# Kernel tuning notes

Hardware: AMD Instinct MI355X
Metric: run time of the kernel (lower is better)

The kernel has to match this reference:

```python
import jax, jax.numpy as jnp
import numpy as np

NUM_EMBEDDINGS = 1024
EMBEDDING_DIM = 256
COMMITMENT_COST = 0.25


def setup_inputs() -> dict:
    key = jax.random.key(0)
    k1, k2 = jax.random.split(key)
    x = jax.random.normal(k1, (16, 4096, EMBEDDING_DIM), dtype=jnp.float32)
    # torch init: uniform(-1/K, 1/K); keep same scale
    embedding_weight = jax.random.uniform(
        k2, (NUM_EMBEDDINGS, EMBEDDING_DIM), dtype=jnp.float32,
        minval=-1.0 / NUM_EMBEDDINGS, maxval=1.0 / NUM_EMBEDDINGS)
    return {"x": x, "embedding_weight": embedding_weight}


def reference(x, embedding_weight):
    original_shape = x.shape
    x_flat = x.reshape(-1, EMBEDDING_DIM)                     # [N, D]
    d2 = (jnp.sum(x_flat ** 2, axis=1, keepdims=True)
          + jnp.sum(embedding_weight ** 2, axis=1)
          - 2.0 * x_flat @ embedding_weight.T)                # [N, K]
    d2 = jnp.maximum(d2, 0.0)
    encoding_indices = jnp.argmin(d2, axis=1)                 # [N]
    quantized_flat = embedding_weight[encoding_indices]        # [N, D]
    quantized = quantized_flat.reshape(original_shape)

    q_sg = jax.lax.stop_gradient(quantized)
    codebook_loss = jnp.mean((q_sg - x) ** 2)
    commitment_loss = jnp.mean((x - q_sg) ** 2)
    vq_total_loss = codebook_loss + COMMITMENT_COST * commitment_loss

    # straight-through estimator
    quantized_st = x + jax.lax.stop_gradient(quantized - x)

    # perplexity via index counts (avoids materializing one-hot [N, K])
    n = x_flat.shape[0]
    counts = jnp.zeros((NUM_EMBEDDINGS,), jnp.float32).at[encoding_indices].add(1.0)
    avg_probs = counts / n
    perplexity = jnp.exp(-jnp.sum(avg_probs * jnp.log(avg_probs + 1e-10)))

    return quantized_st, vq_total_loss, perplexity, encoding_indices
```

## Files before the change

### kernel.cpp

```cpp
#include <hip/hip_runtime.h>
#include <math.h>

#define N_ROWS   65536
#define DIM      256
#define KCODES   1024
#define Q_SIZE   (N_ROWS * DIM)
#define OUT_LOSS Q_SIZE
#define OUT_PERP (Q_SIZE + 1)
#define OUT_IDX  (Q_SIZE + 2)

#define TAUP 200.0f

#define WS_LOSS   0
#define WS_RCNT   8
#define WS_E2     16
#define WS_E2P    4112
#define WS_COUNTS 8208
#define WS_IDX    12304
#define WS_RLIST  274448
#define WS_ET     536592
#define WS_P      1585168

typedef _Float16 half8 __attribute__((ext_vector_type(8)));
typedef _Float16 half4 __attribute__((ext_vector_type(4)));
typedef float    f32x4 __attribute__((ext_vector_type(4)));

#define ROWB 528
#define RPB  128

#define LDS_E2 49152

__global__ void k_prep(const float* __restrict__ E, float* __restrict__ e2,
                       float* __restrict__ e2p, float* __restrict__ Et,
                       _Float16* __restrict__ P,
                       int* __restrict__ counts, double* __restrict__ loss,
                       int* __restrict__ rcnt) {
    int b = blockIdx.x, t = threadIdx.x;
    __shared__ double red[256];
    float v = E[b * DIM + t];
    red[t] = (double)v * (double)v;

    {
        int o    = b * 256 + t;
        int j    = o & 7;
        int lane = (o >> 3) & 63;
        int c    = (o >> 9) & 15;
        int T    = o >> 13;
        int nt = c >> 3, kk = c & 7;
        int code = T * 32 + nt * 16 + (lane & 15);
        int d    = (lane >> 4) * 8 + kk * 32 + j;
        P[o] = (_Float16)(E[code * DIM + d] * 1024.0f);
    }

    __syncthreads();
    for (int s = 128; s > 0; s >>= 1) {
        if (t < s) red[t] += red[t + s];
        __syncthreads();
    }
    if (t == 0) { e2[b] = (float)red[0]; e2p[b] = (float)(red[0] * 1048576.0); }

    int o = b * 256 + t;
    int d = o >> 10, k = o & 1023;
    Et[o] = E[k * DIM + d];

    if (b < 4) counts[b * 256 + t] = 0;
    if (b == 0 && t == 0) { *loss = 0.0; *rcnt = 0; }
}

__global__ void __launch_bounds__(256)
k_main(const float* __restrict__ X, const _Float16* __restrict__ P,
       const float* __restrict__ e2p,
       int* __restrict__ idx_ws, int* __restrict__ rlist,
       int* __restrict__ rcnt) {
    __shared__ __align__(16) char sAll[53248];
    const int tid  = threadIdx.x;
    const int wid  = tid >> 6;
    const int lane = tid & 63;
    const int c16  = lane & 15;
    const int kg   = lane >> 4;
    const int rb   = blockIdx.x * RPB;

    char* sX = sAll;
    char* sB = sAll;
    const float* sE2 = (const float*)(sAll + LDS_E2);

    ((f32x4*)(sAll + LDS_E2))[tid] = ((const f32x4*)e2p)[tid];

    {
        const f32x4* Xg = (const f32x4*)(X + (size_t)rb * DIM);
        #pragma unroll
        for (int it = 0; it < 16; ++it) {
            int f = it * 256 + tid;
            int row = f >> 6, d4 = f & 63;
            f32x4 v = __builtin_nontemporal_load(&Xg[(size_t)row * 64 + d4]);
            half4 hh = {(_Float16)v[0], (_Float16)v[1], (_Float16)v[2], (_Float16)v[3]};
            *(half4*)(sX + row * ROWB + d4 * 8) = hh;
        }
    }
    __syncthreads();
    half8 ar[2][8];
    if (wid < 2) {
        #pragma unroll
        for (int mt = 0; mt < 2; ++mt)
            #pragma unroll
            for (int kk = 0; kk < 8; ++kk)
                ar[mt][kk] = *(const half8*)(sX + (wid * 32 + mt * 16 + c16) * ROWB
                                             + kk * 64 + kg * 16);
    }
    __syncthreads();
    {
        const f32x4* Xg = (const f32x4*)(X + (size_t)(rb + 64) * DIM);
        #pragma unroll
        for (int it = 0; it < 16; ++it) {
            int f = it * 256 + tid;
            int row = f >> 6, d4 = f & 63;
            f32x4 v = __builtin_nontemporal_load(&Xg[(size_t)row * 64 + d4]);
            half4 hh = {(_Float16)v[0], (_Float16)v[1], (_Float16)v[2], (_Float16)v[3]};
            *(half4*)(sX + row * ROWB + d4 * 8) = hh;
        }
    }
    __syncthreads();
    if (wid >= 2) {
        #pragma unroll
        for (int mt = 0; mt < 2; ++mt)
            #pragma unroll
            for (int kk = 0; kk < 8; ++kk)
                ar[mt][kk] = *(const half8*)(sX + ((wid - 2) * 32 + mt * 16 + c16) * ROWB
                                             + kk * 64 + kg * 16);
    }
    __syncthreads();

#define STAGE(T)                                                                             \
    {                                                                                        \
        const char* src_ = (const char*)P + (size_t)(T) * 16384 + (size_t)(wid * 4) * 1024   \
                           + (size_t)lane * 16;                                              \
        char* dst_ = sB + ((T) % 3) * 16384 + (wid * 4) * 1024;                              \
        __builtin_amdgcn_global_load_lds((const __attribute__((address_space(1))) unsigned int*)(src_),          \
                                         (__attribute__((address_space(3))) unsigned int*)(dst_), 16, 0, 0);     \
        __builtin_amdgcn_global_load_lds((const __attribute__((address_space(1))) unsigned int*)(src_ + 1024),   \
                                         (__attribute__((address_space(3))) unsigned int*)(dst_ + 1024), 16, 0, 0);\
        __builtin_amdgcn_global_load_lds((const __attribute__((address_space(1))) unsigned int*)(src_ + 2048),   \
                                         (__attribute__((address_space(3))) unsigned int*)(dst_ + 2048), 16, 0, 0);\
        __builtin_amdgcn_global_load_lds((const __attribute__((address_space(1))) unsigned int*)(src_ + 3072),   \
                                         (__attribute__((address_space(3))) unsigned int*)(dst_ + 3072), 16, 0, 0);\
    }
#define SB0 __builtin_amdgcn_sched_barrier(0)

    float tb1[8], tb2[8];
    int   ti1[8];
    #pragma unroll
    for (int i = 0; i < 8; ++i) { tb1[i] = 3.4e38f; tb2[i] = 3.4e38f; ti1[i] = 0; }

    f32x4 acc[2][2];

    STAGE(0); STAGE(1);
    SB0;

    #pragma unroll 2
    for (int T = 0; T < 32; ++T) {
        if (T <= 30) { asm volatile("s_waitcnt vmcnt(4)" ::: "memory"); }
        else         { asm volatile("s_waitcnt vmcnt(0)" ::: "memory"); }
        SB0;
        __builtin_amdgcn_s_barrier();
        SB0;
        if (T < 30) STAGE(T + 2);
        SB0;

        #pragma unroll
        for (int mt = 0; mt < 2; ++mt)
            #pragma unroll
            for (int nt = 0; nt < 2; ++nt) acc[mt][nt] = 0.0f;

        const char* bbuf = sB + (T % 3) * 16384 + (size_t)lane * 16;
        #pragma unroll
        for (int kk = 0; kk < 8; ++kk) {
            half8 b0 = *(const half8*)(bbuf + (0 * 8 + kk) * 1024);
            half8 b1 = *(const half8*)(bbuf + (1 * 8 + kk) * 1024);
            acc[0][0] = __builtin_amdgcn_mfma_f32_16x16x32_f16(ar[0][kk], b0, acc[0][0], 0, 0, 0);
            acc[0][1] = __builtin_amdgcn_mfma_f32_16x16x32_f16(ar[0][kk], b1, acc[0][1], 0, 0, 0);
            acc[1][0] = __builtin_amdgcn_mfma_f32_16x16x32_f16(ar[1][kk], b0, acc[1][0], 0, 0, 0);
            acc[1][1] = __builtin_amdgcn_mfma_f32_16x16x32_f16(ar[1][kk], b1, acc[1][1], 0, 0, 0);
        }

        #pragma unroll
        for (int nt = 0; nt < 2; ++nt) {
            const int code = T * 32 + nt * 16 + c16;
            const float e2v = sE2[code];
            #pragma unroll
            for (int mt = 0; mt < 2; ++mt)
                #pragma unroll
                for (int r = 0; r < 4; ++r) {
                    float sc = fmaf(-2048.0f, acc[mt][nt][r], e2v);
                    int ix = mt * 4 + r;
                    tb2[ix] = __builtin_amdgcn_fmed3f(tb1[ix], tb2[ix], sc);
                    bool lt = sc < tb1[ix];
                    tb1[ix] = lt ? sc : tb1[ix];
                    ti1[ix] = lt ? code : ti1[ix];
                }
        }
        SB0;
    }
#undef STAGE
#undef SB0

    #pragma unroll
    for (int ix = 0; ix < 8; ++ix) {
        float v1 = tb1[ix], v2 = tb2[ix];
        int   j1 = ti1[ix];
        #pragma unroll
        for (int m = 1; m < 16; m <<= 1) {
            float ov1 = __shfl_xor(v1, m, 64);
            int   oj1 = __shfl_xor(j1, m, 64);
            float ov2 = __shfl_xor(v2, m, 64);
            bool take = (ov1 < v1) || (ov1 == v1 && oj1 < j1);
            float losr = take ? v1 : ov1;
            v1 = take ? ov1 : v1;
            j1 = take ? oj1 : j1;
            v2 = fminf(fminf(v2, ov2), losr);
        }
        tb1[ix] = v1; tb2[ix] = v2; ti1[ix] = j1;
    }
    if (c16 == 0) {
        #pragma unroll
        for (int ix = 0; ix < 8; ++ix) {
            int row = wid * 32 + (ix >> 2) * 16 + kg * 4 + (ix & 3);
            int g = rb + row;
            idx_ws[g] = ti1[ix];
            if (tb2[ix] - tb1[ix] < TAUP) {
                int slot = atomicAdd(rcnt, 1);
                rlist[slot] = g;
            }
        }
    }
}

__launch_bounds__(256, 1)
__global__ void k_refine(const float* __restrict__ X, const float* __restrict__ Et,
                         const float* __restrict__ e2,
                         const int* __restrict__ rlist, const int* __restrict__ rcnt,
                         int* __restrict__ idx_ws) {
    __shared__ float xs[4][256];
    __shared__ float sbv[4][256];
    __shared__ int   sbi[4][256];
    __shared__ float x2s[4];
    __shared__ int   rows[4];
    const int cnt = *rcnt;
    const int t = threadIdx.x;
    for (int base = blockIdx.x * 4; base < cnt; base += gridDim.x * 4) {
        __syncthreads();
        if (t < 4) {
            int e = base + t;
            rows[t] = rlist[e < cnt ? e : (cnt - 1)];
        }
        __syncthreads();
        ((float4*)xs[t >> 6])[t & 63] =
            ((const float4*)(X + (size_t)rows[t >> 6] * DIM))[t & 63];
        __syncthreads();
        if (t < 4) {
            double s = 0.0;
            for (int d = 0; d < DIM; ++d) { double xv = (double)xs[t][d]; s += xv * xv; }
            x2s[t] = (float)s;
        }
        __syncthreads();

        double a0[4], a1[4], a2[4], a3[4];
        #pragma unroll
        for (int r = 0; r < 4; ++r) { a0[r] = 0.0; a1[r] = 0.0; a2[r] = 0.0; a3[r] = 0.0; }
        #pragma unroll 4
        for (int d = 0; d < DIM; ++d) {
            double e0 = (double)Et[d * KCODES + t];
            double e1 = (double)Et[d * KCODES + 256 + t];
            double e2d = (double)Et[d * KCODES + 512 + t];
            double e3 = (double)Et[d * KCODES + 768 + t];
            #pragma unroll
            for (int r = 0; r < 4; ++r) {
                double xv = (double)xs[r][d];
                a0[r] += xv * e0;
                a1[r] += xv * e1;
                a2[r] += xv * e2d;
                a3[r] += xv * e3;
            }
        }

        const float eA = e2[t], eB = e2[256 + t], eC = e2[512 + t], eD = e2[768 + t];
        #pragma unroll
        for (int r = 0; r < 4; ++r) {
            float best = 3.4e38f; int bk = 0;
            float x2 = x2s[r];
            { float d2 = fmaf(-2.f, (float)a0[r], x2 + eA); if (d2 < best) { best = d2; bk = t; } }
            { float d2 = fmaf(-2.f, (float)a1[r], x2 + eB); if (d2 < best) { best = d2; bk = 256 + t; } }
            { float d2 = fmaf(-2.f, (float)a2[r], x2 + eC); if (d2 < best) { best = d2; bk = 512 + t; } }
            { float d2 = fmaf(-2.f, (float)a3[r], x2 + eD); if (d2 < best) { best = d2; bk = 768 + t; } }
            sbv[r][t] = best; sbi[r][t] = bk;
        }
        __syncthreads();
        {
            const int w = t >> 6, lane = t & 63;
            float v = sbv[w][lane];     int id = sbi[w][lane];
            #pragma unroll
            for (int c = 1; c < 4; ++c) {
                float ov = sbv[w][lane + 64 * c]; int oi = sbi[w][lane + 64 * c];
                if (ov < v || (ov == v && oi < id)) { v = ov; id = oi; }
            }
            #pragma unroll
            for (int m = 1; m < 64; m <<= 1) {
                float ov = __shfl_xor(v, m, 64);
                int   oi = __shfl_xor(id, m, 64);
                if (ov < v || (ov == v && oi < id)) { v = ov; id = oi; }
            }
            if (lane == 0 && base + w < cnt) idx_ws[rows[w]] = id;
        }
    }
}

__launch_bounds__(256)
__global__ void k_out(const float* __restrict__ X, const float* __restrict__ E,
                      const int* __restrict__ idx_ws, float* __restrict__ out,
                      int* __restrict__ counts, double* __restrict__ loss) {
    const int tid = threadIdx.x;
    const int w = tid >> 6, lane = tid & 63;
    const int rbase = blockIdx.x * 64;
    double ls = 0.0;
    #pragma unroll 4
    for (int it = 0; it < 16; ++it) {
        const int row = rbase + it * 4 + w;
        const int k = idx_ws[row];
        float4 q = ((const float4*)(E + (size_t)k * DIM))[lane];
        float4 x = ((const float4*)(X + (size_t)row * DIM))[lane];
        ((float4*)(out + (size_t)row * DIM))[lane] = q;
        double d0 = (double)q.x - (double)x.x;
        double d1 = (double)q.y - (double)x.y;
        double d2 = (double)q.z - (double)x.z;
        double d3 = (double)q.w - (double)x.w;
        ls += d0 * d0 + d1 * d1 + d2 * d2 + d3 * d3;
        if (lane == 0) {
            atomicAdd(&counts[k], 1);
            out[OUT_IDX + row] = (float)k;
        }
    }
    __shared__ double red[256];
    red[tid] = ls;
    __syncthreads();
    for (int s = 128; s > 0; s >>= 1) {
        if (tid < s) red[tid] += red[tid + s];
        __syncthreads();
    }
    if (tid == 0) atomicAdd(loss, red[0]);
}

__global__ void k_fin(const int* __restrict__ counts, const double* __restrict__ loss,
                      float* __restrict__ out) {
    int t = threadIdx.x;
    __shared__ double red[256];
    double h = 0.0;
    #pragma unroll
    for (int i = 0; i < 4; ++i) {
        double p = (double)counts[t + i * 256] / (double)N_ROWS;
        h += p * log(p + 1e-10);
    }
    red[t] = h;
    __syncthreads();
    for (int s = 128; s > 0; s >>= 1) {
        if (t < s) red[t] += red[t + s];
        __syncthreads();
    }
    if (t == 0) {
        out[OUT_PERP] = (float)exp(-red[0]);
        out[OUT_LOSS] = (float)((*loss) / (double)Q_SIZE * 1.25);
    }
}

extern "C" void kernel_launch(void* const* d_in, const int* in_sizes, int n_in,
                              void* d_out, int out_size, void* d_ws, size_t ws_size,
                              hipStream_t stream) {
    (void)in_sizes; (void)n_in; (void)out_size; (void)ws_size;
    const float* X = (const float*)d_in[0];
    const float* E = (const float*)d_in[1];
    float* out = (float*)d_out;
    char* ws = (char*)d_ws;

    double*    loss   = (double*)(ws + WS_LOSS);
    int*       rcnt   = (int*)(ws + WS_RCNT);
    float*     e2     = (float*)(ws + WS_E2);
    float*     e2p    = (float*)(ws + WS_E2P);
    int*       counts = (int*)(ws + WS_COUNTS);
    int*       idx_ws = (int*)(ws + WS_IDX);
    int*       rlist  = (int*)(ws + WS_RLIST);
    float*     Et     = (float*)(ws + WS_ET);
    _Float16*  Pp     = (_Float16*)(ws + WS_P);

    k_prep<<<1024, 256, 0, stream>>>(E, e2, e2p, Et, Pp, counts, loss, rcnt);
    k_main<<<N_ROWS / RPB, 256, 0, stream>>>(X, Pp, e2p, idx_ws, rlist, rcnt);
    k_refine<<<1024, 256, 0, stream>>>(X, Et, e2, rlist, rcnt, idx_ws);
    k_out<<<1024, 256, 0, stream>>>(X, E, idx_ws, out, counts, loss);
    k_fin<<<1, 256, 0, stream>>>(counts, loss, out);
}
```

Before: 165.3 us.

## Double rows per block to reuse staged codebook tiles across more rows

Raises rows per block from 128 to 256 so each wave holds 64 rows (4 m-tiles) of X fragments in registers. Each staged codebook tile in LDS is now reused for twice as many MFMAs, halving codebook global traffic and barrier overhead per row. In exchange register pressure doubles for A fragments, accumulators and the top-2 trackers, and the grid halves to 256 blocks, which may underfill the GPU and lengthen the serial X load prologue.

```diff
diff --git a/kernel.cpp b/kernel.cpp
--- a/kernel.cpp
+++ b/kernel.cpp
@@ -26,7 +26,7 @@
 typedef float    f32x4 __attribute__((ext_vector_type(4)));
 
 #define ROWB 528
-#define RPB  128
+#define RPB  256
 
 #define LDS_E2 49152
 
@@ -86,8 +86,10 @@
 
     ((f32x4*)(sAll + LDS_E2))[tid] = ((const f32x4*)e2p)[tid];
 
-    {
-        const f32x4* Xg = (const f32x4*)(X + (size_t)rb * DIM);
+    half8 ar[4][8];
+    #pragma unroll
+    for (int p = 0; p < 4; ++p) {
+        const f32x4* Xg = (const f32x4*)(X + (size_t)(rb + p * 64) * DIM);
         #pragma unroll
         for (int it = 0; it < 16; ++it) {
             int f = it * 256 + tid;
@@ -96,39 +98,17 @@
             half4 hh = {(_Float16)v[0], (_Float16)v[1], (_Float16)v[2], (_Float16)v[3]};
             *(half4*)(sX + row * ROWB + d4 * 8) = hh;
         }
-    }
-    __syncthreads();
-    half8 ar[2][8];
-    if (wid < 2) {
-        #pragma unroll
-        for (int mt = 0; mt < 2; ++mt)
-            #pragma unroll
-            for (int kk = 0; kk < 8; ++kk)
-                ar[mt][kk] = *(const half8*)(sX + (wid * 32 + mt * 16 + c16) * ROWB
-                                             + kk * 64 + kg * 16);
-    }
-    __syncthreads();
-    {
-        const f32x4* Xg = (const f32x4*)(X + (size_t)(rb + 64) * DIM);
-        #pragma unroll
-        for (int it = 0; it < 16; ++it) {
-            int f = it * 256 + tid;
-            int row = f >> 6, d4 = f & 63;
-            f32x4 v = __builtin_nontemporal_load(&Xg[(size_t)row * 64 + d4]);
-            half4 hh = {(_Float16)v[0], (_Float16)v[1], (_Float16)v[2], (_Float16)v[3]};
-            *(half4*)(sX + row * ROWB + d4 * 8) = hh;
-        }
-    }
-    __syncthreads();
-    if (wid >= 2) {
-        #pragma unroll
-        for (int mt = 0; mt < 2; ++mt)
-            #pragma unroll
-            for (int kk = 0; kk < 8; ++kk)
-                ar[mt][kk] = *(const half8*)(sX + ((wid - 2) * 32 + mt * 16 + c16) * ROWB
-                                             + kk * 64 + kg * 16);
-    }
-    __syncthreads();
+        __syncthreads();
+        if (wid == p) {
+            #pragma unroll
+            for (int mt = 0; mt < 4; ++mt)
+                #pragma unroll
+                for (int kk = 0; kk < 8; ++kk)
+                    ar[mt][kk] = *(const half8*)(sX + (mt * 16 + c16) * ROWB
+                                                 + kk * 64 + kg * 16);
+        }
+        __syncthreads();
+    }
 
 #define STAGE(T)                                                                             \
     {                                                                                        \
@@ -146,12 +126,12 @@
     }
 #define SB0 __builtin_amdgcn_sched_barrier(0)
 
-    float tb1[8], tb2[8];
-    int   ti1[8];
+    float tb1[16], tb2[16];
+    int   ti1[16];
     #pragma unroll
-    for (int i = 0; i < 8; ++i) { tb1[i] = 3.4e38f; tb2[i] = 3.4e38f; ti1[i] = 0; }
-
-    f32x4 acc[2][2];
+    for (int i = 0; i < 16; ++i) { tb1[i] = 3.4e38f; tb2[i] = 3.4e38f; ti1[i] = 0; }
+
+    f32x4 acc[4][2];
 
     STAGE(0); STAGE(1);
     SB0;
@@ -167,7 +147,7 @@
         SB0;
 
         #pragma unroll
-        for (int mt = 0; mt < 2; ++mt)
+        for (int mt = 0; mt < 4; ++mt)
             #pragma unroll
             for (int nt = 0; nt < 2; ++nt) acc[mt][nt] = 0.0f;
 
@@ -176,10 +156,11 @@
         for (int kk = 0; kk < 8; ++kk) {
             half8 b0 = *(const half8*)(bbuf + (0 * 8 + kk) * 1024);
             half8 b1 = *(const half8*)(bbuf + (1 * 8 + kk) * 1024);
-            acc[0][0] = __builtin_amdgcn_mfma_f32_16x16x32_f16(ar[0][kk], b0, acc[0][0], 0, 0, 0);
-            acc[0][1] = __builtin_amdgcn_mfma_f32_16x16x32_f16(ar[0][kk], b1, acc[0][1], 0, 0, 0);
-            acc[1][0] = __builtin_amdgcn_mfma_f32_16x16x32_f16(ar[1][kk], b0, acc[1][0], 0, 0, 0);
-            acc[1][1] = __builtin_amdgcn_mfma_f32_16x16x32_f16(ar[1][kk], b1, acc[1][1], 0, 0, 0);
+            #pragma unroll
+            for (int mt = 0; mt < 4; ++mt) {
+                acc[mt][0] = __builtin_amdgcn_mfma_f32_16x16x32_f16(ar[mt][kk], b0, acc[mt][0], 0, 0, 0);
+                acc[mt][1] = __builtin_amdgcn_mfma_f32_16x16x32_f16(ar[mt][kk], b1, acc[mt][1], 0, 0, 0);
+            }
         }
 
         #pragma unroll
@@ -187,7 +168,7 @@
             const int code = T * 32 + nt * 16 + c16;
             const float e2v = sE2[code];
             #pragma unroll
-            for (int mt = 0; mt < 2; ++mt)
+            for (int mt = 0; mt < 4; ++mt)
                 #pragma unroll
                 for (int r = 0; r < 4; ++r) {
                     float sc = fmaf(-2048.0f, acc[mt][nt][r], e2v);
@@ -204,7 +185,7 @@
 #undef SB0
 
     #pragma unroll
-    for (int ix = 0; ix < 8; ++ix) {
+    for (int ix = 0; ix < 16; ++ix) {
         float v1 = tb1[ix], v2 = tb2[ix];
         int   j1 = ti1[ix];
         #pragma unroll
@@ -222,8 +203,8 @@
     }
     if (c16 == 0) {
         #pragma unroll
-        for (int ix = 0; ix < 8; ++ix) {
-            int row = wid * 32 + (ix >> 2) * 16 + kg * 4 + (ix & 3);
+        for (int ix = 0; ix < 16; ++ix) {
+            int row = wid * 64 + (ix >> 2) * 16 + kg * 4 + (ix & 3);
             int g = rb + row;
             idx_ws[g] = ti1[ix];
             if (tb2[ix] - tb1[ix] < TAUP) {
```

After: 179.7 us. +8.7%, slower.

## Split fp64 refine over codebook halves and merge with packed keys

Applied to the files above, without the earlier changes.

The fp64 refinement pass now gives each work unit 8 candidate rows and only half of the codebook. Two units cover each group, and each writes an order-preserving packed (distance, index) 64-bit key for its half. A new merge kernel takes the minimum key per row and writes the final index. This doubles the parallel units and reuses each Et load across 8 rows, at the cost of an extra launch, workspace traffic for the keys, and more LDS per block. hkA reuses the P region that k_main has already finished with.

```diff
diff --git a/kernel.cpp b/kernel.cpp
--- a/kernel.cpp
+++ b/kernel.cpp
@@ -20,6 +20,7 @@
 #define WS_RLIST  274448
 #define WS_ET     536592
 #define WS_P      1585168
+#define WS_HKB    2109456
 
 typedef _Float16 half8 __attribute__((ext_vector_type(8)));
 typedef _Float16 half4 __attribute__((ext_vector_type(4)));
@@ -235,81 +236,109 @@
 }
 
 __launch_bounds__(256, 1)
-__global__ void k_refine(const float* __restrict__ X, const float* __restrict__ Et,
-                         const float* __restrict__ e2,
-                         const int* __restrict__ rlist, const int* __restrict__ rcnt,
-                         int* __restrict__ idx_ws) {
-    __shared__ float xs[4][256];
-    __shared__ float sbv[4][256];
-    __shared__ int   sbi[4][256];
-    __shared__ float x2s[4];
-    __shared__ int   rows[4];
+__global__ void k_rhalf(const float* __restrict__ X, const float* __restrict__ Et,
+                        const float* __restrict__ e2,
+                        const int* __restrict__ rlist, const int* __restrict__ rcnt,
+                        unsigned long long* __restrict__ hkA,
+                        unsigned long long* __restrict__ hkB) {
+    __shared__ float xs[8][256];
+    __shared__ float sbv[8][256];
+    __shared__ int   sbi[8][256];
+    __shared__ float x2s[8];
+    __shared__ int   rows[8];
     const int cnt = *rcnt;
     const int t = threadIdx.x;
-    for (int base = blockIdx.x * 4; base < cnt; base += gridDim.x * 4) {
-        __syncthreads();
-        if (t < 4) {
-            int e = base + t;
+    const int ngroups = (cnt + 7) >> 3;
+    for (int uid = blockIdx.x; uid < 2 * ngroups; uid += gridDim.x) {
+        const int half = uid & 1;
+        const int g8   = uid >> 1;
+        __syncthreads();
+        if (t < 8) {
+            int e = g8 * 8 + t;
             rows[t] = rlist[e < cnt ? e : (cnt - 1)];
         }
         __syncthreads();
-        ((float4*)xs[t >> 6])[t & 63] =
-            ((const float4*)(X + (size_t)rows[t >> 6] * DIM))[t & 63];
-        __syncthreads();
-        if (t < 4) {
+        #pragma unroll
+        for (int i = 0; i < 2; ++i) {
+            int idx = t + i * 256;
+            int r = idx >> 6, c4 = idx & 63;
+            ((float4*)xs[r])[c4] = ((const float4*)(X + (size_t)rows[r] * DIM))[c4];
+        }
+        __syncthreads();
+        if (t < 8) {
             double s = 0.0;
             for (int d = 0; d < DIM; ++d) { double xv = (double)xs[t][d]; s += xv * xv; }
             x2s[t] = (float)s;
         }
         __syncthreads();
 
-        double a0[4], a1[4], a2[4], a3[4];
-        #pragma unroll
-        for (int r = 0; r < 4; ++r) { a0[r] = 0.0; a1[r] = 0.0; a2[r] = 0.0; a3[r] = 0.0; }
+        const int cA = half * 512 + t;
+        const int cB = cA + 256;
+        double a0[8], a1[8];
+        #pragma unroll
+        for (int r = 0; r < 8; ++r) { a0[r] = 0.0; a1[r] = 0.0; }
         #pragma unroll 4
         for (int d = 0; d < DIM; ++d) {
-            double e0 = (double)Et[d * KCODES + t];
-            double e1 = (double)Et[d * KCODES + 256 + t];
-            double e2d = (double)Et[d * KCODES + 512 + t];
-            double e3 = (double)Et[d * KCODES + 768 + t];
-            #pragma unroll
-            for (int r = 0; r < 4; ++r) {
+            double e0 = (double)Et[d * KCODES + cA];
+            double e1 = (double)Et[d * KCODES + cB];
+            #pragma unroll
+            for (int r = 0; r < 8; ++r) {
                 double xv = (double)xs[r][d];
                 a0[r] += xv * e0;
                 a1[r] += xv * e1;
-                a2[r] += xv * e2d;
-                a3[r] += xv * e3;
             }
         }
 
-        const float eA = e2[t], eB = e2[256 + t], eC = e2[512 + t], eD = e2[768 + t];
-        #pragma unroll
-        for (int r = 0; r < 4; ++r) {
-            float best = 3.4e38f; int bk = 0;
+        const float eA = e2[cA], eB = e2[cB];
+        #pragma unroll
+        for (int r = 0; r < 8; ++r) {
             float x2 = x2s[r];
-            { float d2 = fmaf(-2.f, (float)a0[r], x2 + eA); if (d2 < best) { best = d2; bk = t; } }
-            { float d2 = fmaf(-2.f, (float)a1[r], x2 + eB); if (d2 < best) { best = d2; bk = 256 + t; } }
-            { float d2 = fmaf(-2.f, (float)a2[r], x2 + eC); if (d2 < best) { best = d2; bk = 512 + t; } }
-            { float d2 = fmaf(-2.f, (float)a3[r], x2 + eD); if (d2 < best) { best = d2; bk = 768 + t; } }
+            float best; int bk;
+            float d2a = fmaf(-2.f, (float)a0[r], x2 + eA);
+            float d2b = fmaf(-2.f, (float)a1[r], x2 + eB);
+            if (d2a <= d2b) { best = d2a; bk = cA; }
+            else            { best = d2b; bk = cB; }
             sbv[r][t] = best; sbi[r][t] = bk;
         }
         __syncthreads();
         {
             const int w = t >> 6, lane = t & 63;
-            float v = sbv[w][lane];     int id = sbi[w][lane];
-            #pragma unroll
-            for (int c = 1; c < 4; ++c) {
-                float ov = sbv[w][lane + 64 * c]; int oi = sbi[w][lane + 64 * c];
-                if (ov < v || (ov == v && oi < id)) { v = ov; id = oi; }
+            #pragma unroll
+            for (int i = 0; i < 2; ++i) {
+                int r = w * 2 + i;
+                float v = sbv[r][lane];     int id = sbi[r][lane];
+                #pragma unroll
+                for (int c = 1; c < 4; ++c) {
+                    float ov = sbv[r][lane + 64 * c]; int oi = sbi[r][lane + 64 * c];
+                    if (ov < v || (ov == v && oi < id)) { v = ov; id = oi; }
+                }
+                #pragma unroll
+                for (int m = 1; m < 64; m <<= 1) {
+                    float ov = __shfl_xor(v, m, 64);
+                    int   oi = __shfl_xor(id, m, 64);
+                    if (ov < v || (ov == v && oi < id)) { v = ov; id = oi; }
+                }
+                int e = g8 * 8 + r;
+                if (lane == 0 && e < cnt) {
+                    unsigned int u = __float_as_uint(v);
+                    u = (u & 0x80000000u) ? ~u : (u | 0x80000000u);
+                    unsigned long long key = ((unsigned long long)u << 32) | (unsigned int)id;
+                    (half ? hkB : hkA)[e] = key;
+                }
             }
-            #pragma unroll
-            for (int m = 1; m < 64; m <<= 1) {
-                float ov = __shfl_xor(v, m, 64);
-                int   oi = __shfl_xor(id, m, 64);
-                if (ov < v || (ov == v && oi < id)) { v = ov; id = oi; }
-            }
-            if (lane == 0 && base + w < cnt) idx_ws[rows[w]] = id;
-        }
+        }
+    }
+}
+
+__global__ void k_rmerge(const int* __restrict__ rlist, const int* __restrict__ rcnt,
+                         const unsigned long long* __restrict__ hkA,
+                         const unsigned long long* __restrict__ hkB,
+                         int* __restrict__ idx_ws) {
+    int e = blockIdx.x * 256 + threadIdx.x;
+    if (e < *rcnt) {
+        unsigned long long ka = hkA[e], kb = hkB[e];
+        unsigned long long k = ka < kb ? ka : kb;
+        idx_ws[rlist[e]] = (int)(k & 0xFFFFFFFFull);
     }
 }
 
@@ -379,19 +408,22 @@
     float* out = (float*)d_out;
     char* ws = (char*)d_ws;
 
-    double*    loss   = (double*)(ws + WS_LOSS);
-    int*       rcnt   = (int*)(ws + WS_RCNT);
-    float*     e2     = (float*)(ws + WS_E2);
-    float*     e2p    = (float*)(ws + WS_E2P);
-    int*       counts = (int*)(ws + WS_COUNTS);
-    int*       idx_ws = (int*)(ws + WS_IDX);
-    int*       rlist  = (int*)(ws + WS_RLIST);
-    float*     Et     = (float*)(ws + WS_ET);
-    _Float16*  Pp     = (_Float16*)(ws + WS_P);
+    double*             loss   = (double*)(ws + WS_LOSS);
+    int*                rcnt   = (int*)(ws + WS_RCNT);
+    float*              e2     = (float*)(ws + WS_E2);
+    float*              e2p    = (float*)(ws + WS_E2P);
+    int*                counts = (int*)(ws + WS_COUNTS);
+    int*                idx_ws = (int*)(ws + WS_IDX);
+    int*                rlist  = (int*)(ws + WS_RLIST);
+    float*              Et     = (float*)(ws + WS_ET);
+    _Float16*           Pp     = (_Float16*)(ws + WS_P);
+    unsigned long long* hkA    = (unsigned long long*)(ws + WS_P);
+    unsigned long long* hkB    = (unsigned long long*)(ws + WS_HKB);
 
     k_prep<<<1024, 256, 0, stream>>>(E, e2, e2p, Et, Pp, counts, loss, rcnt);
     k_main<<<N_ROWS / RPB, 256, 0, stream>>>(X, Pp, e2p, idx_ws, rlist, rcnt);
-    k_refine<<<1024, 256, 0, stream>>>(X, Et, e2, rlist, rcnt, idx_ws);
+    k_rhalf<<<1024, 256, 0, stream>>>(X, Et, e2, rlist, rcnt, hkA, hkB);
+    k_rmerge<<<256, 256, 0, stream>>>(rlist, rcnt, hkA, hkB, idx_ws);
     k_out<<<1024, 256, 0, stream>>>(X, E, idx_ws, out, counts, loss);
     k_fin<<<1, 256, 0, stream>>>(counts, loss, out);
 }
```

Measured after the change: 186.0 us. 12.5% more time.
